# Performance work log

Hardware: AMD Instinct MI355X
Metric: run time of the kernel (lower is better)

Reference implementation:

```python
import jax, jax.numpy as jnp
import numpy as np

N, E, D, L = 50000, 800000, 128, 3  # nodes, edges, feature dim, num GraphConv layers


def setup_inputs() -> dict:
    key = jax.random.key(0)
    ks = jax.random.split(key, 6)
    x = jax.random.normal(ks[0], (N, D), dtype=jnp.float32)
    edge_index = jax.random.randint(ks[1], (2, E), 0, N, dtype=jnp.int64)
    edge_weight = jax.random.uniform(ks[2], (E,), dtype=jnp.float32)
    s = 1.0 / np.sqrt(D)  # PyG Linear default (kaiming-ish uniform bound)
    W_rel = jax.random.uniform(ks[3], (L, D, D), dtype=jnp.float32, minval=-s, maxval=s)
    b_rel = jax.random.uniform(ks[4], (L, D), dtype=jnp.float32, minval=-s, maxval=s)
    W_root = jax.random.uniform(ks[5], (L, D, D), dtype=jnp.float32, minval=-s, maxval=s)
    return {"x": x, "edge_index": edge_index, "edge_weight": edge_weight,
            "W_rel": W_rel, "b_rel": b_rel, "W_root": W_root}


def reference(x, edge_index, edge_weight, W_rel, b_rel, W_root):
    # PyG GraphConv: out = lin_rel(sum_{j->i} e_ji * x_j) + lin_root(x_i)
    src, dst = edge_index[0], edge_index[1]

    def conv(h, i):
        msg = h[src] * edge_weight[:, None]                     # [E, D] gather + per-edge scale
        agg = jax.ops.segment_sum(msg, dst, num_segments=N)     # [N, D] scatter-add
        return agg @ W_rel[i] + b_rel[i] + h @ W_root[i]

    h = x
    for i in range(L - 1):
        h = jax.nn.relu(conv(h, i))  # dropout is identity at inference
    return conv(h, L - 1)
```

## Files before the change

### kernel.cpp

```cpp
#include <hip/hip_runtime.h>

#define D 128
#define SC_IT 16

typedef __attribute__((ext_vector_type(8))) short bf16x8;
typedef __attribute__((ext_vector_type(4))) float f32x4;
typedef __attribute__((ext_vector_type(4))) int   int4v;

__device__ __forceinline__ float uif(unsigned u) { return __uint_as_float(u); }
__device__ __forceinline__ unsigned short f2bf(float f) {
    unsigned u = __float_as_uint(f);
    u += 0x7fffu + ((u >> 16) & 1u);
    return (unsigned short)(u >> 16);
}
__device__ __forceinline__ float bf2f(unsigned short h) {
    return __uint_as_float(((unsigned)h) << 16);
}

__global__ __launch_bounds__(256) void hist_kernel(
    const int* __restrict__ dst, int* __restrict__ counts, int E)
{
    int base = (blockIdx.x * 256 + threadIdx.x) * 4;
    if (base >= E) return;
    if (base + 4 <= E) {
        int4v d = *(const int4v*)(dst + base);
        atomicAdd(&counts[d.x], 1);
        atomicAdd(&counts[d.y], 1);
        atomicAdd(&counts[d.z], 1);
        atomicAdd(&counts[d.w], 1);
    } else {
        for (int e = base; e < E; ++e) atomicAdd(&counts[dst[e]], 1);
    }
}

__global__ __launch_bounds__(256) void blocksum_kernel(
    const int* __restrict__ counts, int* __restrict__ bsums, int N)
{
    __shared__ int red[256];
    int t = threadIdx.x;
    int i = blockIdx.x * 256 + t;
    red[t] = (i < N) ? counts[i] : 0;
    __syncthreads();
    #pragma unroll
    for (int off = 128; off > 0; off >>= 1) {
        if (t < off) red[t] += red[t + off];
        __syncthreads();
    }
    if (t == 0) bsums[blockIdx.x] = red[0];
}

__global__ __launch_bounds__(256) void scansums_kernel(
    int* __restrict__ bsums, int nb)
{
    __shared__ int s[256];
    int t = threadIdx.x;
    int v = (t < nb) ? bsums[t] : 0;
    s[t] = v;
    __syncthreads();
    #pragma unroll
    for (int off = 1; off < 256; off <<= 1) {
        int tmp = (t >= off) ? s[t - off] : 0;
        __syncthreads();
        s[t] += tmp;
        __syncthreads();
    }
    if (t < nb) bsums[t] = s[t] - v;
}

__global__ __launch_bounds__(256) void emit_kernel(
    const int* __restrict__ counts, const int* __restrict__ bsums,
    int* __restrict__ row_ptr, int* __restrict__ cursor, int N, int E)
{
    __shared__ int s[256];
    int t = threadIdx.x;
    int i = blockIdx.x * 256 + t;
    int v = (i < N) ? counts[i] : 0;
    s[t] = v;
    __syncthreads();
    #pragma unroll
    for (int off = 1; off < 256; off <<= 1) {
        int tmp = (t >= off) ? s[t - off] : 0;
        __syncthreads();
        s[t] += tmp;
        __syncthreads();
    }
    int excl = s[t] - v + bsums[blockIdx.x];
    if (i < N) { row_ptr[i] = excl; cursor[i] = excl; }
    if (blockIdx.x == 0 && t == 0) row_ptr[N] = E;
}

__global__ __launch_bounds__(256) void scatter_xcd_kernel(
    const int* __restrict__ src, const int* __restrict__ dst,
    const float* __restrict__ ew, int* __restrict__ cursor,
    unsigned* __restrict__ edata, int E, int N)
{
    int xcd   = blockIdx.x & 7;
    int chunk = blockIdx.x >> 3;
    int lo = (int)(((long long)xcd * N) >> 3);
    int hi = (int)(((long long)(xcd + 1) * N) >> 3);
    int base = chunk * (256 * SC_IT) + threadIdx.x;
    #pragma unroll
    for (int it = 0; it < SC_IT; ++it) {
        int e = base + it * 256;
        if (e < E) {
            int d = __builtin_nontemporal_load(&dst[e]);
            if (d >= lo && d < hi) {
                int pos = atomicAdd(&cursor[d], 1);
                unsigned pk = (unsigned)(unsigned short)
                                  __builtin_nontemporal_load(&src[e])
                            | ((unsigned)f2bf(
                                  __builtin_nontemporal_load(&ew[e])) << 16);
                edata[pos] = pk;
            }
        }
    }
}

__global__ __launch_bounds__(256) void convert_x_kernel(
    const float* __restrict__ x, short* __restrict__ Ah, int N)
{
    int t = blockIdx.x * 256 + threadIdx.x;
    if (t >= N * 64) return;
    int row = t >> 6;
    int c2  = (t & 63) * 2;
    float2 v = *(const float2*)(x + (size_t)row * D + c2);
    *(unsigned*)(Ah + (size_t)row * D + c2) =
        ((unsigned)f2bf(v.y) << 16) | f2bf(v.x);
}

__global__ __launch_bounds__(256) void convert_w_kernel(
    const float* __restrict__ Wrel, const float* __restrict__ Wroot,
    short* __restrict__ WhiT, short* __restrict__ WloT, int total)
{
    int t = blockIdx.x * 256 + threadIdx.x;
    if (t >= total) return;
    int l = t >> 15;
    int rem = t & 32767;
    int k = rem >> 7;
    int c = rem & 127;
    float f = (k < 128) ? Wrel[(size_t)l * 16384 + k * D + c]
                        : Wroot[(size_t)l * 16384 + (k - 128) * D + c];
    unsigned short h = f2bf(f);
    WhiT[(size_t)l * 32768 + c * 256 + k] = (short)h;
    WloT[(size_t)l * 32768 + c * 256 + k] = (short)f2bf(f - bf2f(h));
}

__global__ __launch_bounds__(256) void gather_bf16(
    const short* __restrict__ Ah, short* __restrict__ aggHi,
    const unsigned* __restrict__ edata, const int* __restrict__ row_ptr, int N)
{
    int wave = (blockIdx.x * 256 + threadIdx.x) >> 6;
    int lane = threadIdx.x & 63;
    if (wave >= N) return;
    int g   = lane >> 4;
    int l16 = lane & 15;
    int beg = row_ptr[wave];
    int cnt = row_ptr[wave + 1] - beg;

    const short* hbase = Ah + l16 * 8;

    float acc[8];
    #pragma unroll
    for (int c = 0; c < 8; ++c) acc[c] = 0.f;

    for (int base = 0; base < cnt; base += 64) {
        int k = base + lane;
        int ed = 0;
        if (k < cnt) ed = (int)edata[beg + k];
        int m = min(64, cnt - base);
        for (int j = 0; j < m; j += 16) {
            int eA = __shfl(ed, j + g);
            int eB = __shfl(ed, j + 4 + g);
            int eC = __shfl(ed, j + 8 + g);
            int eD = __shfl(ed, j + 12 + g);
            float wA = uif((unsigned)eA & 0xffff0000u);
            float wB = uif((unsigned)eB & 0xffff0000u);
            float wC = uif((unsigned)eC & 0xffff0000u);
            float wD = uif((unsigned)eD & 0xffff0000u);
            bf16x8 rA = *(const bf16x8*)(hbase + (size_t)(eA & 0xffff) * D);
            bf16x8 rB = *(const bf16x8*)(hbase + (size_t)(eB & 0xffff) * D);
            bf16x8 rC = *(const bf16x8*)(hbase + (size_t)(eC & 0xffff) * D);
            bf16x8 rD = *(const bf16x8*)(hbase + (size_t)(eD & 0xffff) * D);
            #pragma unroll
            for (int c = 0; c < 8; ++c)
                acc[c] = fmaf(wA, bf2f((unsigned short)rA[c]), acc[c]);
            #pragma unroll
            for (int c = 0; c < 8; ++c)
                acc[c] = fmaf(wB, bf2f((unsigned short)rB[c]), acc[c]);
            #pragma unroll
            for (int c = 0; c < 8; ++c)
                acc[c] = fmaf(wC, bf2f((unsigned short)rC[c]), acc[c]);
            #pragma unroll
            for (int c = 0; c < 8; ++c)
                acc[c] = fmaf(wD, bf2f((unsigned short)rD[c]), acc[c]);
        }
    }

    #pragma unroll
    for (int c = 0; c < 8; ++c) {
        acc[c] += __shfl_xor(acc[c], 16);
        acc[c] += __shfl_xor(acc[c], 32);
    }

    if (g == 0) {
        bf16x8 pk;
        #pragma unroll
        for (int c = 0; c < 8; ++c) pk[c] = (short)f2bf(acc[c]);
        *(bf16x8*)(aggHi + (size_t)wave * D + l16 * 8) = pk;
    }
}

#define STAGE_W(WSRC)                                                           \
    _Pragma("unroll")                                                           \
    for (int r = 0; r < 16; ++r) {                                              \
        int u = r * 256 + tid;                                                  \
        bf16x8 v = *(const bf16x8*)((WSRC) + (size_t)u * 8);                    \
        int scol = u >> 5, sku = u & 31;                                        \
        *(bf16x8*)((char*)bsh + scol * 512 + ((sku ^ (scol & 7)) << 4)) = v;    \
    }

#define MFMA_SEG(APTR, KUOFF)                                                   \
    _Pragma("unroll")                                                           \
    for (int ks = 0; ks < 4; ++ks) {                                            \
        bf16x8 a0 = *(const bf16x8*)((APTR) + aoff0 + ks * 32 + l4 * 8);        \
        bf16x8 a1 = *(const bf16x8*)((APTR) + aoff1 + ks * 32 + l4 * 8);        \
        _Pragma("unroll")                                                       \
        for (int n = 0; n < 4; ++n) {                                           \
            int col = wc * 64 + n * 16 + l15;                                   \
            int ku = (KUOFF) + ks * 4 + l4;                                     \
            bf16x8 b = *(const bf16x8*)((const char*)bsh + col * 512            \
                                        + ((ku ^ (col & 7)) << 4));             \
            acc0[n] = __builtin_amdgcn_mfma_f32_16x16x32_bf16(a0, b, acc0[n], 0, 0, 0); \
            acc1[n] = __builtin_amdgcn_mfma_f32_16x16x32_bf16(a1, b, acc1[n], 0, 0, 0); \
        }                                                                       \
    }

__global__ __launch_bounds__(256, 2) void gemm_mfma(
    const short* __restrict__ aggHi,
    const short* __restrict__ Ah, short* __restrict__ AhN,
    const short* __restrict__ WhiT, const short* __restrict__ WloT,
    const float* __restrict__ bias, float* __restrict__ outf,
    int N, int relu, int writef)
{
    __shared__ short bsh[32768];
    int tid = threadIdx.x;
    int lane = tid & 63;
    int wid = tid >> 6;
    int wr = wid >> 1, wc = wid & 1;
    int l15 = lane & 15, l4 = lane >> 4;
    int row0 = blockIdx.x * 64;

    size_t aoff0 = (size_t)(row0 + wr * 32 + l15) * D;
    size_t aoff1 = aoff0 + 16 * D;

    f32x4 acc0[4], acc1[4];
    #pragma unroll
    for (int n = 0; n < 4; ++n) {
        acc0[n] = (f32x4){0.f, 0.f, 0.f, 0.f};
        acc1[n] = (f32x4){0.f, 0.f, 0.f, 0.f};
    }

    STAGE_W(WhiT);
    __syncthreads();
    MFMA_SEG(aggHi, 0);
    MFMA_SEG(Ah, 16);
    __syncthreads();
    STAGE_W(WloT);
    __syncthreads();
    MFMA_SEG(aggHi, 0);
    MFMA_SEG(Ah, 16);

    #pragma unroll
    for (int n = 0; n < 4; ++n) {
        int col = wc * 64 + n * 16 + l15;
        float bv = bias[col];
        #pragma unroll
        for (int m = 0; m < 2; ++m) {
            f32x4 a = (m == 0) ? acc0[n] : acc1[n];
            #pragma unroll
            for (int r = 0; r < 4; ++r) {
                int row = row0 + wr * 32 + m * 16 + l4 * 4 + r;
                if (row < N) {
                    float v = a[r] + bv;
                    if (relu) v = fmaxf(v, 0.f);
                    if (writef) outf[(size_t)row * D + col] = v;
                    else        AhN[(size_t)row * D + col] = (short)f2bf(v);
                }
            }
        }
    }
}

extern "C" void kernel_launch(void* const* d_in, const int* in_sizes, int n_in,
                              void* d_out, int out_size, void* d_ws, size_t ws_size,
                              hipStream_t stream)
{
    const float* x     = (const float*)d_in[0];
    const int*   ei    = (const int*)d_in[1];
    const float* ew    = (const float*)d_in[2];
    const float* Wrel  = (const float*)d_in[3];
    const float* brel  = (const float*)d_in[4];
    const float* Wroot = (const float*)d_in[5];
    float* out = (float*)d_out;

    int N = in_sizes[0] / D;
    int E = in_sizes[2];
    int L = in_sizes[3] / (D * D);
    int Npad = ((N + 63) / 64) * 64;
    const int* src = ei;
    const int* dst = ei + E;
    int nb = (N + 255) / 256;

    short* Ah0   = (short*)d_ws;
    short* Ah1   = Ah0 + (size_t)Npad * D;
    short* aggHi = Ah1 + (size_t)Npad * D;
    short* WhiT  = aggHi + (size_t)Npad * D;
    short* WloT  = WhiT + (size_t)L * 32768;
    unsigned* edata = (unsigned*)(WloT + (size_t)L * 32768);
    int*   row_ptr = (int*)(edata + E);
    int*   cursor  = row_ptr + (N + 1);
    int*   counts  = cursor + N;
    int*   bsums   = counts + N;

    dim3 blk256(256);
    dim3 grdH((E + 1023) / 1024);
    dim3 grdN(nb);
    int nchunks = (E + 256 * SC_IT - 1) / (256 * SC_IT);
    dim3 grdScat(nchunks * 8);
    dim3 grdGather((N * 64 + 255) / 256);
    dim3 grdGemm(Npad / 64);
    dim3 grdCX((N * 64 + 255) / 256);
    dim3 grdCW((L * 32768 + 255) / 256);

    hipMemsetAsync(counts, 0, (size_t)N * sizeof(int), stream);
    hist_kernel<<<grdH, blk256, 0, stream>>>(dst, counts, E);
    blocksum_kernel<<<grdN, blk256, 0, stream>>>(counts, bsums, N);
    scansums_kernel<<<1, blk256, 0, stream>>>(bsums, nb);
    emit_kernel<<<grdN, blk256, 0, stream>>>(counts, bsums, row_ptr, cursor, N, E);
    scatter_xcd_kernel<<<grdScat, blk256, 0, stream>>>(src, dst, ew, cursor, edata, E, N);

    convert_w_kernel<<<grdCW, blk256, 0, stream>>>(Wrel, Wroot, WhiT, WloT, L * 32768);
    convert_x_kernel<<<grdCX, blk256, 0, stream>>>(x, Ah0, N);

    for (int l = 0; l < L; ++l) {
        const short* Ain  = (l & 1) ? Ah1 : Ah0;
        short*       Aout = (l & 1) ? Ah0 : Ah1;
        gather_bf16<<<grdGather, blk256, 0, stream>>>(Ain, aggHi, edata, row_ptr, N);
        gemm_mfma<<<grdGemm, blk256, 0, stream>>>(
            aggHi, Ain, Aout, WhiT + (size_t)l * 32768, WloT + (size_t)l * 32768,
            brel + (size_t)l * D, out, N, (l < L - 1) ? 1 : 0, (l == L - 1) ? 1 : 0);
    }
}
```

Measured before the change: 278.7 us.

## Use histogram atomic ranks for CSR scatter and enlarge GEMM row tile

The histogram kernel now records the return value of each count atomic as a per-edge rank. The scatter kernel computes each edge's slot as row_ptr plus rank, so it no longer needs a second round of atomics on a cursor array. Separately, the MFMA GEMM tile grows from 64 to 128 rows per block, with each wave computing four 16-row fragments, so each staged weight tile in LDS is reused over more rows. The costs are an extra E-sized rank array of writes and reads, more accumulator registers per wave, and half as many GEMM blocks.

```diff
diff --git a/kernel.cpp b/kernel.cpp
--- a/kernel.cpp
+++ b/kernel.cpp
@@ -17,19 +17,22 @@
     return __uint_as_float(((unsigned)h) << 16);
 }
 
-__global__ __launch_bounds__(256) void hist_kernel(
-    const int* __restrict__ dst, int* __restrict__ counts, int E)
+__global__ __launch_bounds__(256) void rank_kernel(
+    const int* __restrict__ dst, int* __restrict__ counts,
+    int* __restrict__ rank, int E)
 {
     int base = (blockIdx.x * 256 + threadIdx.x) * 4;
     if (base >= E) return;
     if (base + 4 <= E) {
         int4v d = *(const int4v*)(dst + base);
-        atomicAdd(&counts[d.x], 1);
-        atomicAdd(&counts[d.y], 1);
-        atomicAdd(&counts[d.z], 1);
-        atomicAdd(&counts[d.w], 1);
+        int4v r;
+        r.x = atomicAdd(&counts[d.x], 1);
+        r.y = atomicAdd(&counts[d.y], 1);
+        r.z = atomicAdd(&counts[d.z], 1);
+        r.w = atomicAdd(&counts[d.w], 1);
+        *(int4v*)(rank + base) = r;
     } else {
-        for (int e = base; e < E; ++e) atomicAdd(&counts[dst[e]], 1);
+        for (int e = base; e < E; ++e) rank[e] = atomicAdd(&counts[dst[e]], 1);
     }
 }
 
@@ -69,7 +72,7 @@
 
 __global__ __launch_bounds__(256) void emit_kernel(
     const int* __restrict__ counts, const int* __restrict__ bsums,
-    int* __restrict__ row_ptr, int* __restrict__ cursor, int N, int E)
+    int* __restrict__ row_ptr, int N, int E)
 {
     __shared__ int s[256];
     int t = threadIdx.x;
@@ -85,14 +88,14 @@
         __syncthreads();
     }
     int excl = s[t] - v + bsums[blockIdx.x];
-    if (i < N) { row_ptr[i] = excl; cursor[i] = excl; }
+    if (i < N) row_ptr[i] = excl;
     if (blockIdx.x == 0 && t == 0) row_ptr[N] = E;
 }
 
 __global__ __launch_bounds__(256) void scatter_xcd_kernel(
     const int* __restrict__ src, const int* __restrict__ dst,
-    const float* __restrict__ ew, int* __restrict__ cursor,
-    unsigned* __restrict__ edata, int E, int N)
+    const float* __restrict__ ew, const int* __restrict__ row_ptr,
+    const int* __restrict__ rank, unsigned* __restrict__ edata, int E, int N)
 {
     int xcd   = blockIdx.x & 7;
     int chunk = blockIdx.x >> 3;
@@ -105,7 +108,7 @@
         if (e < E) {
             int d = __builtin_nontemporal_load(&dst[e]);
             if (d >= lo && d < hi) {
-                int pos = atomicAdd(&cursor[d], 1);
+                int pos = row_ptr[d] + rank[e];
                 unsigned pk = (unsigned)(unsigned short)
                                   __builtin_nontemporal_load(&src[e])
                             | ((unsigned)f2bf(
@@ -222,16 +225,21 @@
 #define MFMA_SEG(APTR, KUOFF)                                                   \
     _Pragma("unroll")                                                           \
     for (int ks = 0; ks < 4; ++ks) {                                            \
-        bf16x8 a0 = *(const bf16x8*)((APTR) + aoff0 + ks * 32 + l4 * 8);        \
-        bf16x8 a1 = *(const bf16x8*)((APTR) + aoff1 + ks * 32 + l4 * 8);        \
+        bf16x8 av[4];                                                           \
+        _Pragma("unroll")                                                       \
+        for (int m = 0; m < 4; ++m)                                             \
+            av[m] = *(const bf16x8*)((APTR) + abase + (size_t)m * 16 * D        \
+                                     + ks * 32 + l4 * 8);                       \
         _Pragma("unroll")                                                       \
         for (int n = 0; n < 4; ++n) {                                           \
             int col = wc * 64 + n * 16 + l15;                                   \
             int ku = (KUOFF) + ks * 4 + l4;                                     \
             bf16x8 b = *(const bf16x8*)((const char*)bsh + col * 512            \
                                         + ((ku ^ (col & 7)) << 4));             \
-            acc0[n] = __builtin_amdgcn_mfma_f32_16x16x32_bf16(a0, b, acc0[n], 0, 0, 0); \
-            acc1[n] = __builtin_amdgcn_mfma_f32_16x16x32_bf16(a1, b, acc1[n], 0, 0, 0); \
+            _Pragma("unroll")                                                   \
+            for (int m = 0; m < 4; ++m)                                         \
+                acc[m][n] = __builtin_amdgcn_mfma_f32_16x16x32_bf16(            \
+                    av[m], b, acc[m][n], 0, 0, 0);                              \
         }                                                                       \
     }
 
@@ -248,17 +256,16 @@
     int wid = tid >> 6;
     int wr = wid >> 1, wc = wid & 1;
     int l15 = lane & 15, l4 = lane >> 4;
-    int row0 = blockIdx.x * 64;
-
-    size_t aoff0 = (size_t)(row0 + wr * 32 + l15) * D;
-    size_t aoff1 = aoff0 + 16 * D;
-
-    f32x4 acc0[4], acc1[4];
-    #pragma unroll
-    for (int n = 0; n < 4; ++n) {
-        acc0[n] = (f32x4){0.f, 0.f, 0.f, 0.f};
-        acc1[n] = (f32x4){0.f, 0.f, 0.f, 0.f};
-    }
+    int row0 = blockIdx.x * 128;
+
+    size_t abase = (size_t)(row0 + wr * 64 + l15) * D;
+
+    f32x4 acc[4][4];
+    #pragma unroll
+    for (int m = 0; m < 4; ++m)
+        #pragma unroll
+        for (int n = 0; n < 4; ++n)
+            acc[m][n] = (f32x4){0.f, 0.f, 0.f, 0.f};
 
     STAGE_W(WhiT);
     __syncthreads();
@@ -275,13 +282,12 @@
         int col = wc * 64 + n * 16 + l15;
         float bv = bias[col];
         #pragma unroll
-        for (int m = 0; m < 2; ++m) {
-            f32x4 a = (m == 0) ? acc0[n] : acc1[n];
+        for (int m = 0; m < 4; ++m) {
             #pragma unroll
             for (int r = 0; r < 4; ++r) {
-                int row = row0 + wr * 32 + m * 16 + l4 * 4 + r;
+                int row = row0 + wr * 64 + m * 16 + l4 * 4 + r;
                 if (row < N) {
-                    float v = a[r] + bv;
+                    float v = acc[m][n][r] + bv;
                     if (relu) v = fmaxf(v, 0.f);
                     if (writef) outf[(size_t)row * D + col] = v;
                     else        AhN[(size_t)row * D + col] = (short)f2bf(v);
@@ -306,7 +312,7 @@
     int N = in_sizes[0] / D;
     int E = in_sizes[2];
     int L = in_sizes[3] / (D * D);
-    int Npad = ((N + 63) / 64) * 64;
+    int Npad = ((N + 127) / 128) * 128;
     const int* src = ei;
     const int* dst = ei + E;
     int nb = (N + 255) / 256;
@@ -318,8 +324,8 @@
     short* WloT  = WhiT + (size_t)L * 32768;
     unsigned* edata = (unsigned*)(WloT + (size_t)L * 32768);
     int*   row_ptr = (int*)(edata + E);
-    int*   cursor  = row_ptr + (N + 1);
-    int*   counts  = cursor + N;
+    int*   rank    = row_ptr + (N + 1);
+    int*   counts  = rank + E;
     int*   bsums   = counts + N;
 
     dim3 blk256(256);
@@ -328,16 +334,17 @@
     int nchunks = (E + 256 * SC_IT - 1) / (256 * SC_IT);
     dim3 grdScat(nchunks * 8);
     dim3 grdGather((N * 64 + 255) / 256);
-    dim3 grdGemm(Npad / 64);
+    dim3 grdGemm(Npad / 128);
     dim3 grdCX((N * 64 + 255) / 256);
     dim3 grdCW((L * 32768 + 255) / 256);
 
     hipMemsetAsync(counts, 0, (size_t)N * sizeof(int), stream);
-    hist_kernel<<<grdH, blk256, 0, stream>>>(dst, counts, E);
+    rank_kernel<<<grdH, blk256, 0, stream>>>(dst, counts, rank, E);
     blocksum_kernel<<<grdN, blk256, 0, stream>>>(counts, bsums, N);
     scansums_kernel<<<1, blk256, 0, stream>>>(bsums, nb);
-    emit_kernel<<<grdN, blk256, 0, stream>>>(counts, bsums, row_ptr, cursor, N, E);
-    scatter_xcd_kernel<<<grdScat, blk256, 0, stream>>>(src, dst, ew, cursor, edata, E, N);
+    emit_kernel<<<grdN, blk256, 0, stream>>>(counts, bsums, row_ptr, N, E);
+    scatter_xcd_kernel<<<grdScat, blk256, 0, stream>>>(src, dst, ew, row_ptr,
+                                                       rank, edata, E, N);
 
     convert_w_kernel<<<grdCW, blk256, 0, stream>>>(Wrel, Wroot, WhiT, WloT, L * 32768);
     convert_x_kernel<<<grdCX, blk256, 0, stream>>>(x, Ah0, N);
```

Result: faster. 263.3 us (-5.5%).
